# Optimization experiments

Hardware: AMD Instinct MI355X
Metric: run time of the kernel (lower is better)

The kernel has to match this reference:

```python
import jax, jax.numpy as jnp
import numpy as np

H = 64  # hidden size
NUM_GATES = 4


def lstm_layer(x, W_ih, W_hh, b_ih, b_hh):
    """x: [T, B, F] -> ys: [T, B, H]. PyTorch gate order: i, f, g, o."""
    b = b_ih + b_hh

    def step(carry, x_t):
        h, c = carry
        gates = x_t @ W_ih.T + h @ W_hh.T + b  # [B, 4H]
        i, f, g, o = jnp.split(gates, NUM_GATES, axis=-1)
        i = jax.nn.sigmoid(i)
        f = jax.nn.sigmoid(f)
        g = jnp.tanh(g)
        o = jax.nn.sigmoid(o)
        c = f * c + i * g
        h = o * jnp.tanh(c)
        return (h, c), h

    B = x.shape[1]
    h0 = jnp.zeros((B, H), x.dtype)
    (_, _), ys = jax.lax.scan(step, (h0, h0), x)
    return ys


def setup_inputs() -> dict:
    key = jax.random.key(0)
    ks = jax.random.split(key, 16)
    s = 1.0 / np.sqrt(H)  # PyTorch default uniform init bound

    def u(k, shape):
        return jax.random.uniform(k, shape, jnp.float32, -s, s)

    inp = {"x": jax.random.normal(ks[0], (256, 2048, 2), jnp.float32)}
    in_sizes = [2, H, H]
    i = 1
    for l, fin in enumerate(in_sizes):
        inp[f"W_ih{l}"] = u(ks[i], (NUM_GATES * H, fin)); i += 1
        inp[f"W_hh{l}"] = u(ks[i], (NUM_GATES * H, H)); i += 1
        inp[f"b_ih{l}"] = u(ks[i], (NUM_GATES * H,)); i += 1
        inp[f"b_hh{l}"] = u(ks[i], (NUM_GATES * H,)); i += 1
    inp["W_out"] = u(ks[13], (11, H))
    inp["b_out"] = u(ks[14], (11,))
    return inp


def reference(x, W_ih0, W_hh0, b_ih0, b_hh0,
              W_ih1, W_hh1, b_ih1, b_hh1,
              W_ih2, W_hh2, b_ih2, b_hh2,
              W_out, b_out):
    # batch_first -> time-major for scan
    h = jnp.transpose(x, (1, 0, 2))  # [T, B, 2]
    h = lstm_layer(h, W_ih0, W_hh0, b_ih0, b_hh0)
    h = lstm_layer(h, W_ih1, W_hh1, b_ih1, b_hh1)
    h = lstm_layer(h, W_ih2, W_hh2, b_ih2, b_hh2)
    last = h[-1]  # [B, H] == r_out[:, -1, :]
    return last @ W_out.T + b_out  # [B, 11]
```

## Files before the change

kernel.cpp:

```cpp
#include <hip/hip_runtime.h>

#define H 64
#define T_STEPS 2048

typedef _Float16 f16x8 __attribute__((ext_vector_type(8)));
typedef float    f32x4 __attribute__((ext_vector_type(4)));

__device__ __forceinline__ float sig_f(float x) {
    return 1.0f / (1.0f + __expf(-x));
}
__device__ __forceinline__ float tanh_f(float x) {
    return 2.0f / (1.0f + __expf(-2.0f * x)) - 1.0f;
}

__device__ __forceinline__ f16x8 ldcvt8(const float* __restrict__ p) {
    float4 a = ((const float4*)p)[0];
    float4 c = ((const float4*)p)[1];
    f16x8 r;
    r[0]=(_Float16)a.x; r[1]=(_Float16)a.y; r[2]=(_Float16)a.z; r[3]=(_Float16)a.w;
    r[4]=(_Float16)c.x; r[5]=(_Float16)c.y; r[6]=(_Float16)c.z; r[7]=(_Float16)c.w;
    return r;
}

#define MFMA(a, b, c) __builtin_amdgcn_mfma_f32_16x16x32_f16((a), (b), (c), 0, 0, 0)

__global__ __launch_bounds__(1024, 4)
void lstm3_r16(const float* __restrict__ x,
               const float* __restrict__ Wih0, const float* __restrict__ Whh0,
               const float* __restrict__ bih0, const float* __restrict__ bhh0,
               const float* __restrict__ Wih1, const float* __restrict__ Whh1,
               const float* __restrict__ bih1, const float* __restrict__ bhh1,
               const float* __restrict__ Wih2, const float* __restrict__ Whh2,
               const float* __restrict__ bih2, const float* __restrict__ bhh2,
               const float* __restrict__ Wout, const float* __restrict__ bout,
               float* __restrict__ out)
{
    __shared__ __align__(16) float xs[T_STEPS * 2];
    __shared__ __align__(16) _Float16 S[2][384];
    __shared__ __align__(16) float gbuf[3 * H * 4];
    __shared__ __align__(16) float h2f[H];

    const int tid = threadIdx.x;
    const int b   = blockIdx.x;
    const int w   = tid >> 6;
    const int l   = tid & 63;
    const int lj  = l & 15;
    const int kg  = l >> 4;

    ((float4*)xs)[tid] = ((const float4*)(x + (size_t)b * T_STEPS * 2))[tid];

    const int cellA = 4 * w + (lj >> 2);
    const int gateA = lj & 3;
    const int wrow  = gateA * H + cellA;
    const int kc    = kg * 8;

    f16x8 A00 = ldcvt8(Whh0 + wrow * H + kc);
    f16x8 A01 = ldcvt8(Whh0 + wrow * H + 32 + kc);
    f16x8 A10 = ldcvt8(Wih1 + wrow * H + kc);
    f16x8 A11 = ldcvt8(Wih1 + wrow * H + 32 + kc);
    f16x8 A12 = ldcvt8(Whh1 + wrow * H + kc);
    f16x8 A13 = ldcvt8(Whh1 + wrow * H + 32 + kc);
    f16x8 A20 = ldcvt8(Wih2 + wrow * H + kc);
    f16x8 A21 = ldcvt8(Wih2 + wrow * H + 32 + kc);
    f16x8 A22 = ldcvt8(Whh2 + wrow * H + kc);
    f16x8 A23 = ldcvt8(Whh2 + wrow * H + 32 + kc);
    asm volatile("" : "+a"(A00), "+a"(A01), "+a"(A10), "+a"(A11));
    asm volatile("" : "+a"(A12), "+a"(A13), "+a"(A20), "+a"(A21));
    asm volatile("" : "+a"(A22), "+a"(A23));

    float biasv[4], wxv[8];
    float cst = 0.f;
    if (w < 3) {
        const float* bi = (w == 0) ? bih0 : (w == 1) ? bih1 : bih2;
        const float* bh = (w == 0) ? bhh0 : (w == 1) ? bhh1 : bhh2;
#pragma unroll
        for (int g = 0; g < 4; ++g) biasv[g] = bi[g * H + l] + bh[g * H + l];
        if (w == 0) {
#pragma unroll
            for (int g = 0; g < 4; ++g) {
                wxv[2 * g]     = Wih0[(g * H + l) * 2];
                wxv[2 * g + 1] = Wih0[(g * H + l) * 2 + 1];
            }
        }
    }

    if (tid < 384) ((float*)S)[tid] = 0.f;
    __syncthreads();

    const char* Sb  = (const char*)S;
    const int  bofs = (lj == 0) ? (kg * 16) : 384;

    const f32x4 z = {0.f, 0.f, 0.f, 0.f};

#pragma unroll 1
    for (int p = 0; p < T_STEPS + 2; ++p) {
        const int so = ((p + 1) & 1) * 768;
        const char* Bp = Sb + (bofs + so);
        f16x8 b0 = *(const f16x8*)(Bp + 0);
        f16x8 b1 = *(const f16x8*)(Bp + 64);
        f16x8 b2 = *(const f16x8*)(Bp + 128);
        f16x8 b3 = *(const f16x8*)(Bp + 192);
        f16x8 b4 = *(const f16x8*)(Bp + 256);
        f16x8 b5 = *(const f16x8*)(Bp + 320);

        const bool on0 = (p < T_STEPS);
        const bool on1 = (p >= 1) && (p <= T_STEPS);
        const bool on2 = (p >= 2);

        f32x4 g0, g1, g2;
        if (on0) { g0 = MFMA(A00, b0, z);  g0 = MFMA(A01, b1, g0); }
        if (on1) { g1 = MFMA(A10, b0, z);  g1 = MFMA(A11, b1, g1);
                   g1 = MFMA(A12, b2, g1); g1 = MFMA(A13, b3, g1); }
        if (on2) { g2 = MFMA(A20, b2, z);  g2 = MFMA(A21, b3, g2);
                   g2 = MFMA(A22, b4, g2); g2 = MFMA(A23, b5, g2); }

        if (lj == 0) {
            const int ci = 4 * w + kg;
            if (on0) *(f32x4*)&gbuf[(0 * H + ci) * 4] = g0;
            if (on1) *(f32x4*)&gbuf[(1 * H + ci) * 4] = g1;
            if (on2) *(f32x4*)&gbuf[(2 * H + ci) * 4] = g2;
        }
        __syncthreads();

        if (w < 3) {
            const bool on = (w == 0) ? on0 : (w == 1) ? on1 : on2;
            if (on) {
                float4 g = *(const float4*)&gbuf[(w * H + l) * 4];
                float pi = g.x + biasv[0], pf = g.y + biasv[1];
                float pg = g.z + biasv[2], po = g.w + biasv[3];
                if (w == 0) {
                    float2 xt = *(const float2*)&xs[2 * p];
                    pi += wxv[0] * xt.x + wxv[1] * xt.y;
                    pf += wxv[2] * xt.x + wxv[3] * xt.y;
                    pg += wxv[4] * xt.x + wxv[5] * xt.y;
                    po += wxv[6] * xt.x + wxv[7] * xt.y;
                }
                float i_ = sig_f(pi), f_ = sig_f(pf);
                float g_ = tanh_f(pg), o_ = sig_f(po);
                cst = f_ * cst + i_ * g_;
                float hh = o_ * tanh_f(cst);
                S[p & 1][w * H + l] = (_Float16)hh;
                if (w == 2 && p == T_STEPS + 1) h2f[l] = hh;
            }
        }
        __syncthreads();
    }

    if (tid < 11) {
        float acc = bout[tid];
#pragma unroll
        for (int jj = 0; jj < H; ++jj)
            acc += Wout[tid * H + jj] * h2f[jj];
        out[b * 11 + tid] = acc;
    }
}

extern "C" void kernel_launch(void* const* d_in, const int* in_sizes, int n_in,
                              void* d_out, int out_size, void* d_ws, size_t ws_size,
                              hipStream_t stream) {
    const float* x    = (const float*)d_in[0];
    const float* Wih0 = (const float*)d_in[1];
    const float* Whh0 = (const float*)d_in[2];
    const float* bih0 = (const float*)d_in[3];
    const float* bhh0 = (const float*)d_in[4];
    const float* Wih1 = (const float*)d_in[5];
    const float* Whh1 = (const float*)d_in[6];
    const float* bih1 = (const float*)d_in[7];
    const float* bhh1 = (const float*)d_in[8];
    const float* Wih2 = (const float*)d_in[9];
    const float* Whh2 = (const float*)d_in[10];
    const float* bih2 = (const float*)d_in[11];
    const float* bhh2 = (const float*)d_in[12];
    const float* Wout = (const float*)d_in[13];
    const float* bout = (const float*)d_in[14];
    float* out = (float*)d_out;

    lstm3_r16<<<256, 1024, 0, stream>>>(x,
        Wih0, Whh0, bih0, bhh0,
        Wih1, Whh1, bih1, bhh1,
        Wih2, Whh2, bih2, bhh2,
        Wout, bout, out);
}
```

Baseline: 1.855 ms.

## Compute LSTM cell updates in MFMA lanes and drop gate buffer barrier

Removes the shared gate buffer and one of the two per-step block barriers. The lanes that hold the MFMA results for each cell now apply the gate nonlinearities for all three layers directly, keeping three cell states in registers. The four-MFMA accumulation chains are also split into two independent chains that are summed, which shortens the dependent MFMA latency. In exchange, the elementwise work is concentrated in 4 lanes per wave (lj==0) and runs serially across the three layers, and the per-lane register use increases.

```diff
diff --git a/kernel.cpp b/kernel.cpp
--- a/kernel.cpp
+++ b/kernel.cpp
@@ -25,7 +25,7 @@
 #define MFMA(a, b, c) __builtin_amdgcn_mfma_f32_16x16x32_f16((a), (b), (c), 0, 0, 0)
 
 __global__ __launch_bounds__(1024, 4)
-void lstm3_r16(const float* __restrict__ x,
+void lstm3_r17(const float* __restrict__ x,
                const float* __restrict__ Wih0, const float* __restrict__ Whh0,
                const float* __restrict__ bih0, const float* __restrict__ bhh0,
                const float* __restrict__ Wih1, const float* __restrict__ Whh1,
@@ -37,7 +37,6 @@
 {
     __shared__ __align__(16) float xs[T_STEPS * 2];
     __shared__ __align__(16) _Float16 S[2][384];
-    __shared__ __align__(16) float gbuf[3 * H * 4];
     __shared__ __align__(16) float h2f[H];
 
     const int tid = threadIdx.x;
@@ -46,6 +45,7 @@
     const int l   = tid & 63;
     const int lj  = l & 15;
     const int kg  = l >> 4;
+    const int ci  = 4 * w + kg;
 
     ((float4*)xs)[tid] = ((const float4*)(x + (size_t)b * T_STEPS * 2))[tid];
 
@@ -68,32 +68,30 @@
     asm volatile("" : "+a"(A12), "+a"(A13), "+a"(A20), "+a"(A21));
     asm volatile("" : "+a"(A22), "+a"(A23));
 
-    float biasv[4], wxv[8];
-    float cst = 0.f;
-    if (w < 3) {
-        const float* bi = (w == 0) ? bih0 : (w == 1) ? bih1 : bih2;
-        const float* bh = (w == 0) ? bhh0 : (w == 1) ? bhh1 : bhh2;
+    float b0v[4], b1v[4], b2v[4], wxv[8];
 #pragma unroll
-        for (int g = 0; g < 4; ++g) biasv[g] = bi[g * H + l] + bh[g * H + l];
-        if (w == 0) {
-#pragma unroll
-            for (int g = 0; g < 4; ++g) {
-                wxv[2 * g]     = Wih0[(g * H + l) * 2];
-                wxv[2 * g + 1] = Wih0[(g * H + l) * 2 + 1];
-            }
-        }
+    for (int g = 0; g < 4; ++g) {
+        b0v[g] = bih0[g * H + ci] + bhh0[g * H + ci];
+        b1v[g] = bih1[g * H + ci] + bhh1[g * H + ci];
+        b2v[g] = bih2[g * H + ci] + bhh2[g * H + ci];
+        wxv[2 * g]     = Wih0[(g * H + ci) * 2];
+        wxv[2 * g + 1] = Wih0[(g * H + ci) * 2 + 1];
     }
+    float cst0 = 0.f, cst1 = 0.f, cst2 = 0.f;
 
     if (tid < 384) ((float*)S)[tid] = 0.f;
     __syncthreads();
 
     const char* Sb  = (const char*)S;
     const int  bofs = (lj == 0) ? (kg * 16) : 384;
-
     const f32x4 z = {0.f, 0.f, 0.f, 0.f};
 
 #pragma unroll 1
     for (int p = 0; p < T_STEPS + 2; ++p) {
+        const bool on0 = (p < T_STEPS);
+        const bool on1 = (p >= 1) && (p <= T_STEPS);
+        const bool on2 = (p >= 2);
+
         const int so = ((p + 1) & 1) * 768;
         const char* Bp = Sb + (bofs + so);
         f16x8 b0 = *(const f16x8*)(Bp + 0);
@@ -103,44 +101,51 @@
         f16x8 b4 = *(const f16x8*)(Bp + 256);
         f16x8 b5 = *(const f16x8*)(Bp + 320);
 
-        const bool on0 = (p < T_STEPS);
-        const bool on1 = (p >= 1) && (p <= T_STEPS);
-        const bool on2 = (p >= 2);
+        const int px = on0 ? p : 0;
+        float2 xt = *(const float2*)&xs[2 * px];
 
         f32x4 g0, g1, g2;
         if (on0) { g0 = MFMA(A00, b0, z);  g0 = MFMA(A01, b1, g0); }
-        if (on1) { g1 = MFMA(A10, b0, z);  g1 = MFMA(A11, b1, g1);
-                   g1 = MFMA(A12, b2, g1); g1 = MFMA(A13, b3, g1); }
-        if (on2) { g2 = MFMA(A20, b2, z);  g2 = MFMA(A21, b3, g2);
-                   g2 = MFMA(A22, b4, g2); g2 = MFMA(A23, b5, g2); }
+        if (on1) {
+            f32x4 ga = MFMA(A10, b0, z);  ga = MFMA(A11, b1, ga);
+            f32x4 gb = MFMA(A12, b2, z);  gb = MFMA(A13, b3, gb);
+            g1 = ga + gb;
+        }
+        if (on2) {
+            f32x4 ga = MFMA(A20, b2, z);  ga = MFMA(A21, b3, ga);
+            f32x4 gb = MFMA(A22, b4, z);  gb = MFMA(A23, b5, gb);
+            g2 = ga + gb;
+        }
 
         if (lj == 0) {
-            const int ci = 4 * w + kg;
-            if (on0) *(f32x4*)&gbuf[(0 * H + ci) * 4] = g0;
-            if (on1) *(f32x4*)&gbuf[(1 * H + ci) * 4] = g1;
-            if (on2) *(f32x4*)&gbuf[(2 * H + ci) * 4] = g2;
-        }
-        __syncthreads();
-
-        if (w < 3) {
-            const bool on = (w == 0) ? on0 : (w == 1) ? on1 : on2;
-            if (on) {
-                float4 g = *(const float4*)&gbuf[(w * H + l) * 4];
-                float pi = g.x + biasv[0], pf = g.y + biasv[1];
-                float pg = g.z + biasv[2], po = g.w + biasv[3];
-                if (w == 0) {
-                    float2 xt = *(const float2*)&xs[2 * p];
-                    pi += wxv[0] * xt.x + wxv[1] * xt.y;
-                    pf += wxv[2] * xt.x + wxv[3] * xt.y;
-                    pg += wxv[4] * xt.x + wxv[5] * xt.y;
-                    po += wxv[6] * xt.x + wxv[7] * xt.y;
-                }
+            _Float16* Sw = S[p & 1];
+            if (on0) {
+                float pi = g0[0] + b0v[0] + wxv[0] * xt.x + wxv[1] * xt.y;
+                float pf = g0[1] + b0v[1] + wxv[2] * xt.x + wxv[3] * xt.y;
+                float pg = g0[2] + b0v[2] + wxv[4] * xt.x + wxv[5] * xt.y;
+                float po = g0[3] + b0v[3] + wxv[6] * xt.x + wxv[7] * xt.y;
                 float i_ = sig_f(pi), f_ = sig_f(pf);
                 float g_ = tanh_f(pg), o_ = sig_f(po);
-                cst = f_ * cst + i_ * g_;
-                float hh = o_ * tanh_f(cst);
-                S[p & 1][w * H + l] = (_Float16)hh;
-                if (w == 2 && p == T_STEPS + 1) h2f[l] = hh;
+                cst0 = f_ * cst0 + i_ * g_;
+                Sw[ci] = (_Float16)(o_ * tanh_f(cst0));
+            }
+            if (on1) {
+                float pi = g1[0] + b1v[0], pf = g1[1] + b1v[1];
+                float pg = g1[2] + b1v[2], po = g1[3] + b1v[3];
+                float i_ = sig_f(pi), f_ = sig_f(pf);
+                float g_ = tanh_f(pg), o_ = sig_f(po);
+                cst1 = f_ * cst1 + i_ * g_;
+                Sw[H + ci] = (_Float16)(o_ * tanh_f(cst1));
+            }
+            if (on2) {
+                float pi = g2[0] + b2v[0], pf = g2[1] + b2v[1];
+                float pg = g2[2] + b2v[2], po = g2[3] + b2v[3];
+                float i_ = sig_f(pi), f_ = sig_f(pf);
+                float g_ = tanh_f(pg), o_ = sig_f(po);
+                cst2 = f_ * cst2 + i_ * g_;
+                float hh = o_ * tanh_f(cst2);
+                Sw[2 * H + ci] = (_Float16)hh;
+                if (p == T_STEPS + 1) h2f[ci] = hh;
             }
         }
         __syncthreads();
@@ -175,7 +180,7 @@
     const float* bout = (const float*)d_in[14];
     float* out = (float*)d_out;
 
-    lstm3_r16<<<256, 1024, 0, stream>>>(x,
+    lstm3_r17<<<256, 1024, 0, stream>>>(x,
         Wih0, Whh0, bih0, bhh0,
         Wih1, Whh1, bih1, bhh1,
         Wih2, Whh2, bih2, bhh2,
```

Measured after the change: 4.976 ms. 2.68x slower.

## Compute gate nonlinearities in MFMA wave via shuffles, drop gbuf and barrier

Applied to the files above, without the earlier changes.

The gate pre-activations are no longer staged through a shared gbuf with a second __syncthreads. Each wave now gathers its own MFMA outputs with cross-lane shuffles, and 12 lanes per wave do the cell update for 4 cells across the 3 layers. This leaves one barrier per timestep. Bias and the layer-0 input projection are folded into the MFMA accumulator init, and layers 1 and 2 are split into two independent MFMA chains to shorten the dependency. Most lanes do redundant activation math, and all MFMAs now run unconditionally, including the pipeline warm-up and drain steps.

```diff
diff --git a/kernel.cpp b/kernel.cpp
--- a/kernel.cpp
+++ b/kernel.cpp
@@ -25,7 +25,7 @@
 #define MFMA(a, b, c) __builtin_amdgcn_mfma_f32_16x16x32_f16((a), (b), (c), 0, 0, 0)
 
 __global__ __launch_bounds__(1024, 4)
-void lstm3_r16(const float* __restrict__ x,
+void lstm3_r18(const float* __restrict__ x,
                const float* __restrict__ Wih0, const float* __restrict__ Whh0,
                const float* __restrict__ bih0, const float* __restrict__ bhh0,
                const float* __restrict__ Wih1, const float* __restrict__ Whh1,
@@ -37,7 +37,6 @@
 {
     __shared__ __align__(16) float xs[T_STEPS * 2];
     __shared__ __align__(16) _Float16 S[2][384];
-    __shared__ __align__(16) float gbuf[3 * H * 4];
     __shared__ __align__(16) float h2f[H];
 
     const int tid = threadIdx.x;
@@ -68,32 +67,32 @@
     asm volatile("" : "+a"(A12), "+a"(A13), "+a"(A20), "+a"(A21));
     asm volatile("" : "+a"(A22), "+a"(A23));
 
-    float biasv[4], wxv[8];
+    const int cd = 4 * w + kg;
+    f32x4 cb0, cb1, cb2;
+    float wxv[8];
+#pragma unroll
+    for (int r = 0; r < 4; ++r) {
+        cb0[r] = bih0[r * H + cd] + bhh0[r * H + cd];
+        cb1[r] = bih1[r * H + cd] + bhh1[r * H + cd];
+        cb2[r] = bih2[r * H + cd] + bhh2[r * H + cd];
+        wxv[2 * r]     = Wih0[(r * H + cd) * 2];
+        wxv[2 * r + 1] = Wih0[(r * H + cd) * 2 + 1];
+    }
+
+    const int lam  = l >> 2;
+    const int ca   = 4 * w + (l & 3);
+    const int srcl = (l & 3) * 16;
     float cst = 0.f;
-    if (w < 3) {
-        const float* bi = (w == 0) ? bih0 : (w == 1) ? bih1 : bih2;
-        const float* bh = (w == 0) ? bhh0 : (w == 1) ? bhh1 : bhh2;
-#pragma unroll
-        for (int g = 0; g < 4; ++g) biasv[g] = bi[g * H + l] + bh[g * H + l];
-        if (w == 0) {
-#pragma unroll
-            for (int g = 0; g < 4; ++g) {
-                wxv[2 * g]     = Wih0[(g * H + l) * 2];
-                wxv[2 * g + 1] = Wih0[(g * H + l) * 2 + 1];
-            }
-        }
-    }
 
     if (tid < 384) ((float*)S)[tid] = 0.f;
     __syncthreads();
 
     const char* Sb  = (const char*)S;
     const int  bofs = (lj == 0) ? (kg * 16) : 384;
-
     const f32x4 z = {0.f, 0.f, 0.f, 0.f};
 
 #pragma unroll 1
-    for (int p = 0; p < T_STEPS + 2; ++p) {
+    for (int p = 0; p <= T_STEPS + 1; ++p) {
         const int so = ((p + 1) & 1) * 768;
         const char* Bp = Sb + (bofs + so);
         f16x8 b0 = *(const f16x8*)(Bp + 0);
@@ -103,45 +102,41 @@
         f16x8 b4 = *(const f16x8*)(Bp + 256);
         f16x8 b5 = *(const f16x8*)(Bp + 320);
 
-        const bool on0 = (p < T_STEPS);
-        const bool on1 = (p >= 1) && (p <= T_STEPS);
-        const bool on2 = (p >= 2);
+        const int px = (p < T_STEPS) ? p : (T_STEPS - 1);
+        float2 xt = *(const float2*)&xs[2 * px];
+        f32x4 c0;
+#pragma unroll
+        for (int r = 0; r < 4; ++r)
+            c0[r] = cb0[r] + wxv[2 * r] * xt.x + wxv[2 * r + 1] * xt.y;
 
-        f32x4 g0, g1, g2;
-        if (on0) { g0 = MFMA(A00, b0, z);  g0 = MFMA(A01, b1, g0); }
-        if (on1) { g1 = MFMA(A10, b0, z);  g1 = MFMA(A11, b1, g1);
-                   g1 = MFMA(A12, b2, g1); g1 = MFMA(A13, b3, g1); }
-        if (on2) { g2 = MFMA(A20, b2, z);  g2 = MFMA(A21, b3, g2);
-                   g2 = MFMA(A22, b4, g2); g2 = MFMA(A23, b5, g2); }
+        f32x4 g0 = MFMA(A00, b0, c0);  g0 = MFMA(A01, b1, g0);
+        f32x4 ga = MFMA(A10, b0, cb1); ga = MFMA(A11, b1, ga);
+        f32x4 gb = MFMA(A12, b2, z);   gb = MFMA(A13, b3, gb);
+        f32x4 g1 = ga + gb;
+        f32x4 gc = MFMA(A20, b2, cb2); gc = MFMA(A21, b3, gc);
+        f32x4 gd = MFMA(A22, b4, z);   gd = MFMA(A23, b5, gd);
+        f32x4 g2 = gc + gd;
 
-        if (lj == 0) {
-            const int ci = 4 * w + kg;
-            if (on0) *(f32x4*)&gbuf[(0 * H + ci) * 4] = g0;
-            if (on1) *(f32x4*)&gbuf[(1 * H + ci) * 4] = g1;
-            if (on2) *(f32x4*)&gbuf[(2 * H + ci) * 4] = g2;
-        }
-        __syncthreads();
+        float u0 = __shfl(g0[0], srcl), u1 = __shfl(g0[1], srcl);
+        float u2 = __shfl(g0[2], srcl), u3 = __shfl(g0[3], srcl);
+        float v0 = __shfl(g1[0], srcl), v1 = __shfl(g1[1], srcl);
+        float v2 = __shfl(g1[2], srcl), v3 = __shfl(g1[3], srcl);
+        float t0 = __shfl(g2[0], srcl), t1 = __shfl(g2[1], srcl);
+        float t2 = __shfl(g2[2], srcl), t3 = __shfl(g2[3], srcl);
+        float pi = (lam == 0) ? u0 : (lam == 1) ? v0 : t0;
+        float pf = (lam == 0) ? u1 : (lam == 1) ? v1 : t1;
+        float pg = (lam == 0) ? u2 : (lam == 1) ? v2 : t2;
+        float po = (lam == 0) ? u3 : (lam == 1) ? v3 : t3;
 
-        if (w < 3) {
-            const bool on = (w == 0) ? on0 : (w == 1) ? on1 : on2;
-            if (on) {
-                float4 g = *(const float4*)&gbuf[(w * H + l) * 4];
-                float pi = g.x + biasv[0], pf = g.y + biasv[1];
-                float pg = g.z + biasv[2], po = g.w + biasv[3];
-                if (w == 0) {
-                    float2 xt = *(const float2*)&xs[2 * p];
-                    pi += wxv[0] * xt.x + wxv[1] * xt.y;
-                    pf += wxv[2] * xt.x + wxv[3] * xt.y;
-                    pg += wxv[4] * xt.x + wxv[5] * xt.y;
-                    po += wxv[6] * xt.x + wxv[7] * xt.y;
-                }
-                float i_ = sig_f(pi), f_ = sig_f(pf);
-                float g_ = tanh_f(pg), o_ = sig_f(po);
-                cst = f_ * cst + i_ * g_;
-                float hh = o_ * tanh_f(cst);
-                S[p & 1][w * H + l] = (_Float16)hh;
-                if (w == 2 && p == T_STEPS + 1) h2f[l] = hh;
-            }
+        float i_ = sig_f(pi), f_ = sig_f(pf);
+        float g_ = tanh_f(pg), o_ = sig_f(po);
+        float cn = f_ * cst + i_ * g_;
+        float hh = o_ * tanh_f(cn);
+        const bool vact = (l < 12) && (p >= lam) && (p < T_STEPS + lam);
+        if (vact) {
+            cst = cn;
+            S[p & 1][lam * H + ca] = (_Float16)hh;
+            if (lam == 2 && p == T_STEPS + 1) h2f[ca] = hh;
         }
         __syncthreads();
     }
@@ -175,7 +170,7 @@
     const float* bout = (const float*)d_in[14];
     float* out = (float*)d_out;
 
-    lstm3_r16<<<256, 1024, 0, stream>>>(x,
+    lstm3_r18<<<256, 1024, 0, stream>>>(x,
         Wih0, Whh0, bih0, bhh0,
         Wih1, Whh1, bih1, bhh1,
         Wih2, Whh2, bih2, bhh2,
```

Result: slower. 2.702 ms (+45.7%).
